# Optimization experiments

Hardware: AMD Instinct MI355X
Metric: run time of the kernel (lower is better)

The kernel has to match this reference:

```python
import jax, jax.numpy as jnp
import numpy as np

N = 50000      # nodes
E = 800000     # edges (avg degree 16)
IN = 256       # input feature dim
HID = 128      # hidden dim
H = 4          # heads
C = HID // H   # per-head dim = 32
L = 3          # layers


def setup_inputs() -> dict:
    key = jax.random.key(0)
    ks = jax.random.split(key, 16)
    s = 0.02
    f32 = jnp.float32
    inp = {
        "x": jax.random.normal(ks[0], (N, IN), f32),
        "edge_index": jax.random.randint(ks[1], (2, E), 0, N, dtype=jnp.int32),
        "edge_attr": jax.random.normal(ks[2], (E, 1), f32),
        "Wi": jax.random.normal(ks[3], (IN, HID), f32) * s,
        "bi": jnp.zeros((HID,), f32),
        "Wq": jax.random.normal(ks[4], (L, HID, HID), f32) * s,
        "bq": jnp.zeros((L, HID), f32),
        "Wk": jax.random.normal(ks[5], (L, HID, HID), f32) * s,
        "bk": jnp.zeros((L, HID), f32),
        "Wv": jax.random.normal(ks[6], (L, HID, HID), f32) * s,
        "bv": jnp.zeros((L, HID), f32),
        "We": jax.random.normal(ks[7], (L, 1, HID), f32) * s,      # lin_edge, no bias
        "Wskip": jax.random.normal(ks[8], (L, HID, HID), f32) * s,
        "bskip": jnp.zeros((L, HID), f32),
        "Wbeta": jax.random.normal(ks[9], (L, 3 * HID, 1), f32) * s,  # lin_beta, no bias
        "ln_g": jnp.ones((L, HID), f32),
        "ln_b": jnp.zeros((L, HID), f32),
    }
    return inp


def _layer_norm(x, g, b, eps=1e-5):
    mu = jnp.mean(x, axis=-1, keepdims=True)
    var = jnp.var(x, axis=-1, keepdims=True)
    return (x - mu) * jax.lax.rsqrt(var + eps) * g + b


def _transformer_conv(h, src, dst, edge_attr, Wq, bq, Wk, bk, Wv, bv, We, Wskip, bskip, Wbeta):
    # node-level projections [N, HID]
    q = h @ Wq + bq
    k = h @ Wk + bk
    v = h @ Wv + bv
    e = edge_attr @ We                       # [E, HID] edge embedding
    # per-edge gathered features [E, H, C]
    qi = q[dst].reshape(E, H, C)
    kj = (k[src] + e).reshape(E, H, C)
    vj = (v[src] + e).reshape(E, H, C)
    # attention logits [E, H]
    alpha = jnp.sum(qi * kj, axis=-1) / np.sqrt(C)
    # segment softmax over destination node
    amax = jax.ops.segment_max(alpha, dst, num_segments=N)   # [N, H]
    ex = jnp.exp(alpha - amax[dst])
    denom = jax.ops.segment_sum(ex, dst, num_segments=N)     # [N, H]
    attn = ex / (denom[dst] + 1e-16)                         # [E, H]
    # scatter-add aggregation -> [N, H, C] -> concat heads [N, HID]
    out = jax.ops.segment_sum(attn[..., None] * vj, dst, num_segments=N).reshape(N, HID)
    # gated skip (beta=True, root_weight=True)
    x_r = h @ Wskip + bskip
    beta = jax.nn.sigmoid(jnp.concatenate([out, x_r, out - x_r], axis=-1) @ Wbeta)  # [N, 1]
    return beta * x_r + (1.0 - beta) * out


def reference(x, edge_index, edge_attr, Wi, bi, Wq, bq, Wk, bk, Wv, bv, We, Wskip, bskip, Wbeta, ln_g, ln_b):
    src = edge_index[0]
    dst = edge_index[1]
    h = x @ Wi + bi
    for l in range(L):
        res = h
        h = _transformer_conv(h, src, dst, edge_attr,
                              Wq[l], bq[l], Wk[l], bk[l], Wv[l], bv[l],
                              We[l], Wskip[l], bskip[l], Wbeta[l])
        h = jax.nn.gelu(h, approximate=False)
        h = _layer_norm(h + res, ln_g[l], ln_b[l])
        # dropout: eval mode -> identity
    return h
```

## Files before the change

kernel.cpp:

```cpp
#include <hip/hip_runtime.h>
#include <math.h>

#define NNODES 50000
#define NEDGES 800000
#define DIN 256
#define DHID 128

typedef __attribute__((ext_vector_type(8))) short short8;
typedef __attribute__((ext_vector_type(4))) float f32x4;
typedef __attribute__((ext_vector_type(2))) float f32x2;

__device__ __forceinline__ unsigned short f2bf(float f) {
    unsigned u = __builtin_bit_cast(unsigned, f);
    u += 0x7fffu + ((u >> 16) & 1u);
    return (unsigned short)(u >> 16);
}
__device__ __forceinline__ float bf2f(unsigned short s) {
    return __builtin_bit_cast(float, (unsigned)s << 16);
}
__device__ __forceinline__ unsigned packbf(float a, float b) {
    return (unsigned)f2bf(a) | ((unsigned)f2bf(b) << 16);
}
__device__ __forceinline__ float dpp_xor1(float x) {
    return __builtin_bit_cast(float, __builtin_amdgcn_update_dpp(0, __builtin_bit_cast(int, x), 0xB1, 0xF, 0xF, true));
}
__device__ __forceinline__ float dpp_xor2(float x) {
    return __builtin_bit_cast(float, __builtin_amdgcn_update_dpp(0, __builtin_bit_cast(int, x), 0x4E, 0xF, 0xF, true));
}
__device__ __forceinline__ float dpp_hmirror(float x) {
    return __builtin_bit_cast(float, __builtin_amdgcn_update_dpp(0, __builtin_bit_cast(int, x), 0x141, 0xF, 0xF, true));
}
__device__ __forceinline__ float dpp_mirror(float x) {
    return __builtin_bit_cast(float, __builtin_amdgcn_update_dpp(0, __builtin_bit_cast(int, x), 0x140, 0xF, 0xF, true));
}
__device__ __forceinline__ float red16(float x) {
    x += dpp_xor1(x);
    x += dpp_xor2(x);
    x += dpp_hmirror(x);
    x += dpp_mirror(x);
    return x;
}

__global__ __launch_bounds__(256) void k_hist(const int* __restrict__ dst, int* __restrict__ counts) {
    int e = blockIdx.x * 256 + threadIdx.x;
    if (e < NEDGES) atomicAdd(&counts[dst[e]], 1);
}

__global__ __launch_bounds__(256) void k_scan_block(const int* __restrict__ in, int* __restrict__ out,
                                                    int* __restrict__ partials, int n) {
    __shared__ int sh[256];
    int tid = threadIdx.x;
    int i = blockIdx.x * 256 + tid;
    int vv = (i < n) ? in[i] : 0;
    sh[tid] = vv;
    __syncthreads();
    for (int off = 1; off < 256; off <<= 1) {
        int t = (tid >= off) ? sh[tid - off] : 0;
        __syncthreads();
        sh[tid] += t;
        __syncthreads();
    }
    if (i < n) out[i] = sh[tid];
    if (tid == 255) partials[blockIdx.x] = sh[255];
}

__global__ __launch_bounds__(256) void k_apply2(const int* __restrict__ partials, int* __restrict__ row_ptr, int n,
                                                int nb) {
    __shared__ int sh[256];
    int tid = threadIdx.x;
    int vv = (tid < nb) ? partials[tid] : 0;
    sh[tid] = vv;
    __syncthreads();
    for (int off = 1; off < 256; off <<= 1) {
        int t = (tid >= off) ? sh[tid - off] : 0;
        __syncthreads();
        sh[tid] += t;
        __syncthreads();
    }
    int i = blockIdx.x * 256 + tid;
    if (i < n) {
        int add = blockIdx.x ? sh[blockIdx.x - 1] : 0;
        row_ptr[i + 1] += add;
    }
    if (i == 0) row_ptr[0] = 0;
}

__global__ __launch_bounds__(256) void k_scatter(const int* __restrict__ src, const int* __restrict__ dst,
                                                 const float* __restrict__ ea, const int* __restrict__ row_ptr,
                                                 int* __restrict__ fill, int2* __restrict__ esrc) {
    int e = blockIdx.x * 256 + threadIdx.x;
    if (e < NEDGES) {
        int d = dst[e];
        int old = atomicSub(&fill[d], 1);
        int pos = row_ptr[d] + old - 1;
        esrc[pos] = make_int2(src[e], __float_as_int(ea[e]));
    }
}

__global__ __launch_bounds__(256) void prep_w(const float* __restrict__ Wi, const float* __restrict__ Wq,
                                              const float* __restrict__ Wk, const float* __restrict__ Wv,
                                              const float* __restrict__ Ws, unsigned short* __restrict__ Wit,
                                              unsigned short* __restrict__ Wt3) {
    int idx = blockIdx.x * 256 + threadIdx.x;
    if (idx < DHID * DIN) {
        int n = idx >> 8, kk = idx & 255;
        Wit[idx] = f2bf(Wi[kk * DHID + n]);
    }
    int idx2 = idx - DHID * DIN;
    if (idx2 >= 0 && idx2 < 3 * 512 * DHID) {
        int l = idx2 / (512 * DHID);
        int rem = idx2 - l * 512 * DHID;
        int r = rem >> 7;
        int kk = rem & 127;
        int sel = r >> 7, rl = r & 127;
        const float* srcm = sel == 0 ? Wq : sel == 1 ? Wk : sel == 2 ? Wv : Ws;
        Wt3[idx2] = f2bf(srcm[l * DHID * DHID + kk * DHID + rl]);
    }
}

__global__ __launch_bounds__(256) void gemm_in(const float* __restrict__ A, const unsigned short* __restrict__ Wt,
                                               const float* __restrict__ bias, unsigned* __restrict__ h32, int M) {
    __shared__ short As[128 * 128];
    const int tid = threadIdx.x;
    const int lane = tid & 63;
    const int wid = tid >> 6;
    const int row0 = blockIdx.x * 128;
    const int wr = (wid & 1) * 64;
    const int wc = (wid >> 1) * 64;
    f32x4 acc[4][4] = {};
    const int srow = tid >> 1;
    const int sk = (tid & 1) * 64;
    const int grow = min(row0 + srow, M - 1);
    for (int kt = 0; kt < 2; ++kt) {
        const float* ap = A + (size_t)grow * DIN + kt * 128 + sk;
#pragma unroll
        for (int i = 0; i < 8; ++i) {
            float4 f0 = *(const float4*)(ap + i * 8);
            float4 f1 = *(const float4*)(ap + i * 8 + 4);
            short8 s;
            s[0] = f2bf(f0.x); s[1] = f2bf(f0.y); s[2] = f2bf(f0.z); s[3] = f2bf(f0.w);
            s[4] = f2bf(f1.x); s[5] = f2bf(f1.y); s[6] = f2bf(f1.z); s[7] = f2bf(f1.w);
            int g = (sk >> 3) + i;
            *(short8*)(&As[srow * 128 + ((g ^ (srow & 7)) << 3)]) = s;
        }
        __syncthreads();
#pragma unroll
        for (int ks = 0; ks < 4; ++ks) {
            short8 a[4], b[4];
#pragma unroll
            for (int m = 0; m < 4; ++m) {
                int r = wr + m * 16 + (lane & 15);
                int g = ks * 4 + (lane >> 4);
                a[m] = *(const short8*)(&As[r * 128 + ((g ^ (r & 7)) << 3)]);
            }
#pragma unroll
            for (int n = 0; n < 4; ++n) {
                int c = wc + n * 16 + (lane & 15);
                b[n] = *(const short8*)(Wt + (size_t)c * DIN + kt * 128 + ks * 32 + (lane >> 4) * 8);
            }
#pragma unroll
            for (int m = 0; m < 4; ++m)
#pragma unroll
                for (int n = 0; n < 4; ++n)
                    acc[m][n] = __builtin_amdgcn_mfma_f32_16x16x32_bf16(a[m], b[n], acc[m][n], 0, 0, 0);
        }
        __syncthreads();
    }
    float* my = ((float*)As) + wid * 1024;
    float bb[4];
#pragma unroll
    for (int n = 0; n < 4; ++n) bb[n] = bias[wc + n * 16 + (lane & 15)];
    const int rr = lane >> 2;
    const int cb = lane & 3;
#pragma unroll
    for (int m = 0; m < 4; ++m) {
#pragma unroll
        for (int n = 0; n < 4; ++n) {
            int lc = n * 16 + (lane & 15);
#pragma unroll
            for (int j = 0; j < 4; ++j) {
                int row = (lane >> 4) * 4 + j;
                my[row * 64 + (((lc >> 2) ^ (row & 7)) << 2) + (lc & 3)] = acc[m][n][j] + bb[n];
            }
        }
        float vals[16];
#pragma unroll
        for (int s = 0; s < 4; ++s) {
            int gx = (cb * 4 + s) ^ (rr & 7);
            f32x4 t4 = *(const f32x4*)(my + rr * 64 + gx * 4);
            vals[s * 4 + 0] = t4.x; vals[s * 4 + 1] = t4.y; vals[s * 4 + 2] = t4.z; vals[s * 4 + 3] = t4.w;
        }
        int grow2 = row0 + wr + m * 16 + rr;
        if (grow2 < M) {
            unsigned pk[8];
#pragma unroll
            for (int d = 0; d < 8; ++d) pk[d] = packbf(vals[2 * d], vals[2 * d + 1]);
            unsigned* op = h32 + (size_t)grow2 * 64 + (wc >> 1) + cb * 8;
            *(uint4*)op = make_uint4(pk[0], pk[1], pk[2], pk[3]);
            *(uint4*)(op + 4) = make_uint4(pk[4], pk[5], pk[6], pk[7]);
        }
    }
}

__global__ __launch_bounds__(512) void gemm_qkvs(const unsigned short* __restrict__ A,
                                                 const unsigned short* __restrict__ Wt, const float* __restrict__ bq,
                                                 const float* __restrict__ bk, const float* __restrict__ bv,
                                                 const float* __restrict__ bs, unsigned* __restrict__ q32,
                                                 unsigned* __restrict__ kv, unsigned* __restrict__ xr32, int M) {
    __shared__ short As[128 * 128];
    const int tid = threadIdx.x;
    const int lane = tid & 63;
    const int wid = tid >> 6;
    const int row0 = blockIdx.x * 128;
    const int sel = wid >> 2;
    const int wr = (wid & 1) * 64;
    const int wc = ((wid >> 1) & 1) * 64;
    f32x4 acc0[4][4] = {}, acc1[4][4] = {};
    {
        const int srow = tid >> 2;
        const int sk = (tid & 3) * 32;
        const int grow = min(row0 + srow, M - 1);
        const unsigned short* ap = A + (size_t)grow * DHID + sk;
#pragma unroll
        for (int i = 0; i < 4; ++i) {
            short8 s = *(const short8*)(ap + i * 8);
            int g = (sk >> 3) + i;
            *(short8*)(&As[srow * 128 + ((g ^ (srow & 7)) << 3)]) = s;
        }
    }
    __syncthreads();
    const int b0base = sel ? 128 : 0;
    const int b1base = sel ? 256 : 384;
#pragma unroll
    for (int ks = 0; ks < 4; ++ks) {
        short8 a[4], b0[4], b1[4];
#pragma unroll
        for (int m = 0; m < 4; ++m) {
            int r = wr + m * 16 + (lane & 15);
            int g = ks * 4 + (lane >> 4);
            a[m] = *(const short8*)(&As[r * 128 + ((g ^ (r & 7)) << 3)]);
        }
#pragma unroll
        for (int n = 0; n < 4; ++n) {
            int rb = wc + n * 16 + (lane & 15);
            b0[n] = *(const short8*)(Wt + (size_t)(b0base + rb) * DHID + ks * 32 + (lane >> 4) * 8);
            b1[n] = *(const short8*)(Wt + (size_t)(b1base + rb) * DHID + ks * 32 + (lane >> 4) * 8);
        }
#pragma unroll
        for (int m = 0; m < 4; ++m)
#pragma unroll
            for (int n = 0; n < 4; ++n) {
                acc0[m][n] = __builtin_amdgcn_mfma_f32_16x16x32_bf16(a[m], b0[n], acc0[m][n], 0, 0, 0);
                acc1[m][n] = __builtin_amdgcn_mfma_f32_16x16x32_bf16(a[m], b1[n], acc1[m][n], 0, 0, 0);
            }
    }
    __syncthreads();
    float* my = ((float*)As) + wid * 1024;
    const float* bias0 = sel ? bk : bq;
    const float* bias1 = sel ? bv : bs;
    float bb0[4], bb1[4];
#pragma unroll
    for (int n = 0; n < 4; ++n) {
        int c = wc + n * 16 + (lane & 15);
        bb0[n] = bias0[c];
        bb1[n] = bias1[c];
    }
    const int rr = lane >> 2;
    const int cb = lane & 3;
#pragma unroll
    for (int m = 0; m < 4; ++m) {
        float vals0[16], vals1[16];
#pragma unroll
        for (int n = 0; n < 4; ++n) {
            int lc = n * 16 + (lane & 15);
#pragma unroll
            for (int j = 0; j < 4; ++j) {
                int row = (lane >> 4) * 4 + j;
                my[row * 64 + (((lc >> 2) ^ (row & 7)) << 2) + (lc & 3)] = acc0[m][n][j] + bb0[n];
            }
        }
#pragma unroll
        for (int s = 0; s < 4; ++s) {
            int gx = (cb * 4 + s) ^ (rr & 7);
            f32x4 t4 = *(const f32x4*)(my + rr * 64 + gx * 4);
            vals0[s * 4 + 0] = t4.x; vals0[s * 4 + 1] = t4.y; vals0[s * 4 + 2] = t4.z; vals0[s * 4 + 3] = t4.w;
        }
#pragma unroll
        for (int n = 0; n < 4; ++n) {
            int lc = n * 16 + (lane & 15);
#pragma unroll
            for (int j = 0; j < 4; ++j) {
                int row = (lane >> 4) * 4 + j;
                my[row * 64 + (((lc >> 2) ^ (row & 7)) << 2) + (lc & 3)] = acc1[m][n][j] + bb1[n];
            }
        }
#pragma unroll
        for (int s = 0; s < 4; ++s) {
            int gx = (cb * 4 + s) ^ (rr & 7);
            f32x4 t4 = *(const f32x4*)(my + rr * 64 + gx * 4);
            vals1[s * 4 + 0] = t4.x; vals1[s * 4 + 1] = t4.y; vals1[s * 4 + 2] = t4.z; vals1[s * 4 + 3] = t4.w;
        }
        int grow2 = row0 + wr + m * 16 + rr;
        if (grow2 < M) {
            size_t obase = (size_t)grow2 * 64 + (wc >> 1) + cb * 8;
            if (sel == 0) {
                unsigned p0[8], p1[8];
#pragma unroll
                for (int d = 0; d < 8; ++d) {
                    p0[d] = packbf(vals0[2 * d], vals0[2 * d + 1]);
                    p1[d] = packbf(vals1[2 * d], vals1[2 * d + 1]);
                }
                *(uint4*)(q32 + obase) = make_uint4(p0[0], p0[1], p0[2], p0[3]);
                *(uint4*)(q32 + obase + 4) = make_uint4(p0[4], p0[5], p0[6], p0[7]);
                *(uint4*)(xr32 + obase) = make_uint4(p1[0], p1[1], p1[2], p1[3]);
                *(uint4*)(xr32 + obase + 4) = make_uint4(p1[4], p1[5], p1[6], p1[7]);
            } else {
                unsigned pk[8];
#pragma unroll
                for (int d = 0; d < 8; ++d) {
                    unsigned u = (unsigned)__builtin_amdgcn_cvt_pk_fp8_f32(vals0[2 * d], vals0[2 * d + 1], 0, false);
                    u = (unsigned)__builtin_amdgcn_cvt_pk_fp8_f32(vals1[2 * d], vals1[2 * d + 1], (int)u, true);
                    pk[d] = u;
                }
                *(uint4*)(kv + obase) = make_uint4(pk[0], pk[1], pk[2], pk[3]);
                *(uint4*)(kv + obase + 4) = make_uint4(pk[4], pk[5], pk[6], pk[7]);
            }
        }
    }
}

__global__ __launch_bounds__(256) void node_attn_fuse(const unsigned* __restrict__ q32,
                                                      const unsigned* __restrict__ kv, const int2* __restrict__ esrc,
                                                      const float* __restrict__ We, const int* __restrict__ row_ptr,
                                                      const unsigned* __restrict__ xr32, const unsigned* res32,
                                                      const float* __restrict__ Wb, const float* __restrict__ lng,
                                                      const float* __restrict__ lnb, unsigned* houtb, float* houtf) {
    const int tid = threadIdx.x;
    const int lane = tid & 63;
    const int lnl = lane & 15;
    const int gbase = lane & 48;
    const int node = blockIdx.x * 16 + (tid >> 4);
    const int base = row_ptr[node], end = row_ptr[node + 1];
    const float SC = 0.25505654047688565f;
    const float THR = 8.0f;

    float qv[8], wev[8];
    {
        uint4 qw = *(const uint4*)(q32 + (size_t)node * 64 + 4 * lnl);
        unsigned qd[4] = {qw.x, qw.y, qw.z, qw.w};
#pragma unroll
        for (int t = 0; t < 4; ++t) {
            qv[2 * t] = bf2f((unsigned short)qd[t]) * SC;
            qv[2 * t + 1] = bf2f((unsigned short)(qd[t] >> 16)) * SC;
        }
        float4 wlo = *(const float4*)(We + 8 * lnl);
        float4 whi = *(const float4*)(We + 8 * lnl + 4);
        wev[0] = wlo.x; wev[1] = wlo.y; wev[2] = wlo.z; wev[3] = wlo.w;
        wev[4] = whi.x; wev[5] = whi.y; wev[6] = whi.z; wev[7] = whi.w;
    }
    float qwe;
    {
        float s = 0.f;
#pragma unroll
        for (int i = 0; i < 8; ++i) s = fmaf(qv[i], wev[i], s);
        s += dpp_xor1(s);
        s += dpp_xor2(s);
        qwe = s;
    }

    float m = -1e30f, sden = 0.f, tacc = 0.f;
    float acc[8] = {};
    const unsigned* kvp = kv + 4 * lnl;

    for (int off = 0; ; off += 16) {
        int cnt = min(end - base - off, 16);
        if (__all(cnt <= 0)) break;
        int s_l = 0;
        float a_l = 0.f;
        if (lnl < cnt) {
            int2 sa = esrc[base + off + lnl];
            s_l = sa.x;
            a_l = __int_as_float(sa.y);
        }
        int cm = max(cnt, 0);
        cm = max(cm, __shfl_xor(cm, 16));
        cm = max(cm, __shfl_xor(cm, 32));
        int src_n = __shfl(s_l, gbase);
        float av_n = __shfl(a_l, gbase);
        uint4 kw_n = *(const uint4*)(kvp + (size_t)src_n * 64);
        for (int j = 0; j < cm; ++j) {
            uint4 kw = kw_n;
            float av = av_n;
            bool valid = j < cnt;
            if (j + 1 < cm) {
                int src1 = __shfl(s_l, gbase + j + 1);
                av_n = __shfl(a_l, gbase + j + 1);
                kw_n = *(const uint4*)(kvp + (size_t)src1 * 64);
            }
            unsigned kd[4] = {kw.x, kw.y, kw.z, kw.w};
            float vj[8];
            float p = 0.f;
#pragma unroll
            for (int t = 0; t < 4; ++t) {
                f32x2 kk = __builtin_amdgcn_cvt_pk_f32_fp8((int)kd[t], false);
                f32x2 vv = __builtin_amdgcn_cvt_pk_f32_fp8((int)kd[t], true);
                p = fmaf(qv[2 * t], kk.x, p);
                p = fmaf(qv[2 * t + 1], kk.y, p);
                vj[2 * t] = vv.x;
                vj[2 * t + 1] = vv.y;
            }
            p += dpp_xor1(p);
            p += dpp_xor2(p);
            p = fmaf(av, qwe, p);
            p = valid ? p : -3e38f;
            if (__any(p - m > THR)) {
                float mn2 = fmaxf(m, p);
                float wgt = exp2f(p - mn2);
                float sc = exp2f(m - mn2);
                sden = fmaf(sden, sc, wgt);
                tacc = fmaf(tacc, sc, wgt * av);
#pragma unroll
                for (int i = 0; i < 8; ++i) acc[i] = fmaf(acc[i], sc, wgt * vj[i]);
                m = mn2;
            } else {
                float wgt = exp2f(p - m);
                sden += wgt;
                tacc = fmaf(wgt, av, tacc);
#pragma unroll
                for (int i = 0; i < 8; ++i) acc[i] = fmaf(wgt, vj[i], acc[i]);
            }
        }
    }

    float rden = 1.f / (sden + 1e-16f);
    float o[8];
#pragma unroll
    for (int i = 0; i < 8; ++i) o[i] = fmaf(tacc, wev[i], acc[i]) * rden;

    float x[8];
    {
        uint4 xw = *(const uint4*)(xr32 + (size_t)node * 64 + 4 * lnl);
        unsigned xd[4] = {xw.x, xw.y, xw.z, xw.w};
#pragma unroll
        for (int t = 0; t < 4; ++t) {
            x[2 * t] = bf2f((unsigned short)xd[t]);
            x[2 * t + 1] = bf2f((unsigned short)(xd[t] >> 16));
        }
    }
    float bl = 0.f;
#pragma unroll
    for (int t = 0; t < 2; ++t) {
        float4 w0 = *(const float4*)(Wb + 8 * lnl + 4 * t);
        float4 w1 = *(const float4*)(Wb + 128 + 8 * lnl + 4 * t);
        float4 w2 = *(const float4*)(Wb + 256 + 8 * lnl + 4 * t);
        bl = fmaf(o[4 * t], w0.x, bl); bl = fmaf(o[4 * t + 1], w0.y, bl);
        bl = fmaf(o[4 * t + 2], w0.z, bl); bl = fmaf(o[4 * t + 3], w0.w, bl);
        bl = fmaf(x[4 * t], w1.x, bl); bl = fmaf(x[4 * t + 1], w1.y, bl);
        bl = fmaf(x[4 * t + 2], w1.z, bl); bl = fmaf(x[4 * t + 3], w1.w, bl);
        bl = fmaf(o[4 * t] - x[4 * t], w2.x, bl); bl = fmaf(o[4 * t + 1] - x[4 * t + 1], w2.y, bl);
        bl = fmaf(o[4 * t + 2] - x[4 * t + 2], w2.z, bl); bl = fmaf(o[4 * t + 3] - x[4 * t + 3], w2.w, bl);
    }
    bl = red16(bl);
    float beta = 1.f / (1.f + __expf(-bl));
    float tpre[8];
    {
        uint4 rw = *(const uint4*)(res32 + (size_t)node * 64 + 4 * lnl);
        unsigned rd[4] = {rw.x, rw.y, rw.z, rw.w};
#pragma unroll
        for (int i = 0; i < 8; ++i) {
            float gg = beta * x[i] + (1.f - beta) * o[i];
            gg = 0.5f * gg * (1.f + erff(gg * 0.70710678118654752f));
            float rv = (i & 1) ? bf2f((unsigned short)(rd[i >> 1] >> 16)) : bf2f((unsigned short)rd[i >> 1]);
            tpre[i] = gg + rv;
        }
    }
    float su = 0.f, sq = 0.f;
#pragma unroll
    for (int i = 0; i < 8; ++i) {
        su += tpre[i];
        sq = fmaf(tpre[i], tpre[i], sq);
    }
    su = red16(su);
    sq = red16(sq);
    float mu = su * (1.f / 128.f);
    float var = sq * (1.f / 128.f) - mu * mu;
    float inv = rsqrtf(var + 1e-5f);
    float4 g0 = *(const float4*)(lng + 8 * lnl);
    float4 g1 = *(const float4*)(lng + 8 * lnl + 4);
    float4 b0 = *(const float4*)(lnb + 8 * lnl);
    float4 b1 = *(const float4*)(lnb + 8 * lnl + 4);
    float gg[8] = {g0.x, g0.y, g0.z, g0.w, g1.x, g1.y, g1.z, g1.w};
    float bb[8] = {b0.x, b0.y, b0.z, b0.w, b1.x, b1.y, b1.z, b1.w};
    float ov[8];
#pragma unroll
    for (int i = 0; i < 8; ++i) ov[i] = (tpre[i] - mu) * inv * gg[i] + bb[i];
    if (houtf) {
        float* op = houtf + (size_t)node * 128 + 8 * lnl;
        *(float4*)op = make_float4(ov[0], ov[1], ov[2], ov[3]);
        *(float4*)(op + 4) = make_float4(ov[4], ov[5], ov[6], ov[7]);
    } else {
        unsigned pk[4];
#pragma unroll
        for (int d = 0; d < 4; ++d) pk[d] = packbf(ov[2 * d], ov[2 * d + 1]);
        *(uint4*)(houtb + (size_t)node * 64 + 4 * lnl) = make_uint4(pk[0], pk[1], pk[2], pk[3]);
    }
}

extern "C" void kernel_launch(void* const* d_in, const int* in_sizes, int n_in, void* d_out, int out_size,
                              void* d_ws, size_t ws_size, hipStream_t stream) {
    const float* x = (const float*)d_in[0];
    const int* ei = (const int*)d_in[1];
    const float* ea = (const float*)d_in[2];
    const float* Wi = (const float*)d_in[3];
    const float* bi = (const float*)d_in[4];
    const float* Wq = (const float*)d_in[5];
    const float* bq = (const float*)d_in[6];
    const float* Wk = (const float*)d_in[7];
    const float* bk = (const float*)d_in[8];
    const float* Wv = (const float*)d_in[9];
    const float* bv = (const float*)d_in[10];
    const float* We = (const float*)d_in[11];
    const float* Wskip = (const float*)d_in[12];
    const float* bskip = (const float*)d_in[13];
    const float* Wbeta = (const float*)d_in[14];
    const float* lng = (const float*)d_in[15];
    const float* lnb = (const float*)d_in[16];

    const int* srcp = ei;
    const int* dstp = ei + NEDGES;

    char* p = (char*)d_ws;
    auto alloc = [&](size_t bytes) {
        void* r = (void*)p;
        p += (bytes + 255) & ~(size_t)255;
        return r;
    };
    unsigned* h32 = (unsigned*)alloc((size_t)NNODES * 64 * 4);
    unsigned* q32 = (unsigned*)alloc((size_t)NNODES * 64 * 4);
    unsigned* xr32 = (unsigned*)alloc((size_t)NNODES * 64 * 4);
    unsigned* kv = (unsigned*)alloc((size_t)NNODES * 64 * 4);
    unsigned short* Wit = (unsigned short*)alloc((size_t)DHID * DIN * 2);
    unsigned short* Wt3 = (unsigned short*)alloc((size_t)3 * 512 * DHID * 2);
    int* counts = (int*)alloc((size_t)NNODES * 4);
    int* row_ptr = (int*)alloc((size_t)(NNODES + 1) * 4);
    int2* esrc = (int2*)alloc((size_t)NEDGES * 8);
    int* partials = (int*)alloc(256 * 4);

    const int EB = (NEDGES + 255) / 256;
    const int NB = (NNODES + 255) / 256;
    const int GB = (NNODES + 127) / 128;
    const int WB = NNODES / 16;
    const int PB = (DHID * DIN + 3 * 512 * DHID + 255) / 256;

    prep_w<<<PB, 256, 0, stream>>>(Wi, Wq, Wk, Wv, Wskip, Wit, Wt3);

    hipMemsetAsync(counts, 0, (size_t)NNODES * 4, stream);
    k_hist<<<EB, 256, 0, stream>>>(dstp, counts);
    k_scan_block<<<NB, 256, 0, stream>>>(counts, row_ptr + 1, partials, NNODES);
    k_apply2<<<NB, 256, 0, stream>>>(partials, row_ptr, NNODES, NB);
    k_scatter<<<EB, 256, 0, stream>>>(srcp, dstp, ea, row_ptr, counts, esrc);

    gemm_in<<<GB, 256, 0, stream>>>(x, Wit, bi, h32, NNODES);

    for (int l = 0; l < 3; ++l) {
        const size_t bo = (size_t)l * 128;
        gemm_qkvs<<<GB, 512, 0, stream>>>((const unsigned short*)h32, Wt3 + (size_t)l * 512 * DHID, bq + bo, bk + bo,
                                          bv + bo, bskip + bo, q32, kv, xr32, NNODES);
        node_attn_fuse<<<WB, 256, 0, stream>>>(q32, kv, esrc, We + bo, row_ptr, xr32, h32,
                                               Wbeta + (size_t)l * 384, lng + bo, lnb + bo, h32,
                                               (l == 2) ? (float*)d_out : nullptr);
    }
}
```

Measured before the change: 330.4 us.

## Fuse setup kernels and pack edge records into 32-bit src/bf16 attr

Merges weight prep with the degree histogram, and the CSR scatter with the input GEMM, into single launches whose blocks branch by role. This removes launch gaps and lets the independent work run side by side. Edge records shrink from an int2 to one 32-bit word: a 16-bit source index plus a bf16 edge attribute. That halves the edge-list traffic read by the attention kernel in every layer, and the scatter uses nontemporal stores. The cost is reduced precision for edge_attr, and the layout only works while the node count stays below 65536.

```diff
diff --git a/kernel.cpp b/kernel.cpp
--- a/kernel.cpp
+++ b/kernel.cpp
@@ -5,6 +5,7 @@
 #define NEDGES 800000
 #define DIN 256
 #define DHID 128
+#define GBLK 391
 
 typedef __attribute__((ext_vector_type(8))) short short8;
 typedef __attribute__((ext_vector_type(4))) float f32x4;
@@ -41,9 +42,31 @@
     return x;
 }
 
-__global__ __launch_bounds__(256) void k_hist(const int* __restrict__ dst, int* __restrict__ counts) {
-    int e = blockIdx.x * 256 + threadIdx.x;
-    if (e < NEDGES) atomicAdd(&counts[dst[e]], 1);
+__global__ __launch_bounds__(256) void prep_hist(const float* __restrict__ Wi, const float* __restrict__ Wq,
+                                                 const float* __restrict__ Wk, const float* __restrict__ Wv,
+                                                 const float* __restrict__ Ws, unsigned short* __restrict__ Wit,
+                                                 unsigned short* __restrict__ Wt3, const int* __restrict__ dst,
+                                                 int* __restrict__ counts, int pb) {
+    if ((int)blockIdx.x < pb) {
+        int idx = blockIdx.x * 256 + threadIdx.x;
+        if (idx < DHID * DIN) {
+            int n = idx >> 8, kk = idx & 255;
+            Wit[idx] = f2bf(Wi[kk * DHID + n]);
+        }
+        int idx2 = idx - DHID * DIN;
+        if (idx2 >= 0 && idx2 < 3 * 512 * DHID) {
+            int l = idx2 / (512 * DHID);
+            int rem = idx2 - l * 512 * DHID;
+            int r = rem >> 7;
+            int kk = rem & 127;
+            int sel = r >> 7, rl = r & 127;
+            const float* srcm = sel == 0 ? Wq : sel == 1 ? Wk : sel == 2 ? Wv : Ws;
+            Wt3[idx2] = f2bf(srcm[l * DHID * DHID + kk * DHID + rl]);
+        }
+    } else {
+        int e = (blockIdx.x - pb) * 256 + threadIdx.x;
+        if (e < NEDGES) atomicAdd(&counts[dst[e]], 1);
+    }
 }
 
 __global__ __launch_bounds__(256) void k_scan_block(const int* __restrict__ in, int* __restrict__ out,
@@ -85,43 +108,24 @@
     if (i == 0) row_ptr[0] = 0;
 }
 
-__global__ __launch_bounds__(256) void k_scatter(const int* __restrict__ src, const int* __restrict__ dst,
-                                                 const float* __restrict__ ea, const int* __restrict__ row_ptr,
-                                                 int* __restrict__ fill, int2* __restrict__ esrc) {
-    int e = blockIdx.x * 256 + threadIdx.x;
-    if (e < NEDGES) {
-        int d = dst[e];
-        int old = atomicSub(&fill[d], 1);
-        int pos = row_ptr[d] + old - 1;
-        esrc[pos] = make_int2(src[e], __float_as_int(ea[e]));
-    }
-}
-
-__global__ __launch_bounds__(256) void prep_w(const float* __restrict__ Wi, const float* __restrict__ Wq,
-                                              const float* __restrict__ Wk, const float* __restrict__ Wv,
-                                              const float* __restrict__ Ws, unsigned short* __restrict__ Wit,
-                                              unsigned short* __restrict__ Wt3) {
-    int idx = blockIdx.x * 256 + threadIdx.x;
-    if (idx < DHID * DIN) {
-        int n = idx >> 8, kk = idx & 255;
-        Wit[idx] = f2bf(Wi[kk * DHID + n]);
-    }
-    int idx2 = idx - DHID * DIN;
-    if (idx2 >= 0 && idx2 < 3 * 512 * DHID) {
-        int l = idx2 / (512 * DHID);
-        int rem = idx2 - l * 512 * DHID;
-        int r = rem >> 7;
-        int kk = rem & 127;
-        int sel = r >> 7, rl = r & 127;
-        const float* srcm = sel == 0 ? Wq : sel == 1 ? Wk : sel == 2 ? Wv : Ws;
-        Wt3[idx2] = f2bf(srcm[l * DHID * DHID + kk * DHID + rl]);
-    }
-}
-
-__global__ __launch_bounds__(256) void gemm_in(const float* __restrict__ A, const unsigned short* __restrict__ Wt,
-                                               const float* __restrict__ bias, unsigned* __restrict__ h32, int M) {
+__global__ __launch_bounds__(256) void scatter_gemm(const float* __restrict__ A, const unsigned short* __restrict__ Wt,
+                                                    const float* __restrict__ bias, unsigned* __restrict__ h32, int M,
+                                                    const int* __restrict__ src, const int* __restrict__ dst,
+                                                    const float* __restrict__ ea, const int* __restrict__ row_ptr,
+                                                    int* __restrict__ fill, unsigned* __restrict__ esrc) {
     __shared__ short As[128 * 128];
     const int tid = threadIdx.x;
+    if ((int)blockIdx.x >= GBLK) {
+        int e = (blockIdx.x - GBLK) * 256 + tid;
+        if (e < NEDGES) {
+            int d = dst[e];
+            int old = atomicSub(&fill[d], 1);
+            int pos = row_ptr[d] + old - 1;
+            unsigned pk = (unsigned)src[e] | ((unsigned)f2bf(ea[e]) << 16);
+            __builtin_nontemporal_store(pk, &esrc[pos]);
+        }
+        return;
+    }
     const int lane = tid & 63;
     const int wid = tid >> 6;
     const int row0 = blockIdx.x * 128;
@@ -330,7 +334,7 @@
 }
 
 __global__ __launch_bounds__(256) void node_attn_fuse(const unsigned* __restrict__ q32,
-                                                      const unsigned* __restrict__ kv, const int2* __restrict__ esrc,
+                                                      const unsigned* __restrict__ kv, const unsigned* __restrict__ esrc,
                                                       const float* __restrict__ We, const int* __restrict__ row_ptr,
                                                       const unsigned* __restrict__ xr32, const unsigned* res32,
                                                       const float* __restrict__ Wb, const float* __restrict__ lng,
@@ -375,27 +379,20 @@
     for (int off = 0; ; off += 16) {
         int cnt = min(end - base - off, 16);
         if (__all(cnt <= 0)) break;
-        int s_l = 0;
-        float a_l = 0.f;
-        if (lnl < cnt) {
-            int2 sa = esrc[base + off + lnl];
-            s_l = sa.x;
-            a_l = __int_as_float(sa.y);
-        }
+        unsigned u_l = 0;
+        if (lnl < cnt) u_l = esrc[base + off + lnl];
         int cm = max(cnt, 0);
         cm = max(cm, __shfl_xor(cm, 16));
         cm = max(cm, __shfl_xor(cm, 32));
-        int src_n = __shfl(s_l, gbase);
-        float av_n = __shfl(a_l, gbase);
-        uint4 kw_n = *(const uint4*)(kvp + (size_t)src_n * 64);
+        unsigned ue_n = __shfl((int)u_l, gbase);
+        uint4 kw_n = *(const uint4*)(kvp + (size_t)(ue_n & 0xFFFFu) * 64);
         for (int j = 0; j < cm; ++j) {
             uint4 kw = kw_n;
-            float av = av_n;
+            float av = bf2f((unsigned short)(ue_n >> 16));
             bool valid = j < cnt;
             if (j + 1 < cm) {
-                int src1 = __shfl(s_l, gbase + j + 1);
-                av_n = __shfl(a_l, gbase + j + 1);
-                kw_n = *(const uint4*)(kvp + (size_t)src1 * 64);
+                ue_n = __shfl((int)u_l, gbase + j + 1);
+                kw_n = *(const uint4*)(kvp + (size_t)(ue_n & 0xFFFFu) * 64);
             }
             unsigned kd[4] = {kw.x, kw.y, kw.z, kw.w};
             float vj[8];
@@ -543,29 +540,24 @@
     unsigned short* Wt3 = (unsigned short*)alloc((size_t)3 * 512 * DHID * 2);
     int* counts = (int*)alloc((size_t)NNODES * 4);
     int* row_ptr = (int*)alloc((size_t)(NNODES + 1) * 4);
-    int2* esrc = (int2*)alloc((size_t)NEDGES * 8);
+    unsigned* esrc = (unsigned*)alloc((size_t)NEDGES * 4);
     int* partials = (int*)alloc(256 * 4);
 
     const int EB = (NEDGES + 255) / 256;
     const int NB = (NNODES + 255) / 256;
-    const int GB = (NNODES + 127) / 128;
     const int WB = NNODES / 16;
     const int PB = (DHID * DIN + 3 * 512 * DHID + 255) / 256;
 
-    prep_w<<<PB, 256, 0, stream>>>(Wi, Wq, Wk, Wv, Wskip, Wit, Wt3);
-
     hipMemsetAsync(counts, 0, (size_t)NNODES * 4, stream);
-    k_hist<<<EB, 256, 0, stream>>>(dstp, counts);
+    prep_hist<<<PB + EB, 256, 0, stream>>>(Wi, Wq, Wk, Wv, Wskip, Wit, Wt3, dstp, counts, PB);
     k_scan_block<<<NB, 256, 0, stream>>>(counts, row_ptr + 1, partials, NNODES);
     k_apply2<<<NB, 256, 0, stream>>>(partials, row_ptr, NNODES, NB);
-    k_scatter<<<EB, 256, 0, stream>>>(srcp, dstp, ea, row_ptr, counts, esrc);
-
-    gemm_in<<<GB, 256, 0, stream>>>(x, Wit, bi, h32, NNODES);
+    scatter_gemm<<<GBLK + EB, 256, 0, stream>>>(x, Wit, bi, h32, NNODES, srcp, dstp, ea, row_ptr, counts, esrc);
 
     for (int l = 0; l < 3; ++l) {
         const size_t bo = (size_t)l * 128;
-        gemm_qkvs<<<GB, 512, 0, stream>>>((const unsigned short*)h32, Wt3 + (size_t)l * 512 * DHID, bq + bo, bk + bo,
-                                          bv + bo, bskip + bo, q32, kv, xr32, NNODES);
+        gemm_qkvs<<<GBLK, 512, 0, stream>>>((const unsigned short*)h32, Wt3 + (size_t)l * 512 * DHID, bq + bo, bk + bo,
+                                            bv + bo, bskip + bo, q32, kv, xr32, NNODES);
         node_attn_fuse<<<WB, 256, 0, stream>>>(q32, kv, esrc, We + bo, row_ptr, xr32, h32,
                                                Wbeta + (size_t)l * 384, lng + bo, lnb + bo, h32,
                                                (l == 2) ? (float*)d_out : nullptr);
```

Result: no change. 325.8 us (-1.4%).
